# Performance work log

Measured on AMD Instinct MI355X. Metric: run time of the kernel, lower is better.

## Reference

```python
import jax, jax.numpy as jnp
import numpy as np

B, S, E = 4, 2048, 1024
H, DK = 16, 64

def setup_inputs() -> dict:
    key = jax.random.key(0)
    ks = jax.random.split(key, 9)
    sc = 1.0 / np.sqrt(E)
    return {
        "q": jax.random.normal(ks[0], (B, S, E), jnp.float32),
        "Wq": jax.random.normal(ks[1], (E, H * DK), jnp.float32) * sc,
        "bq": jax.random.normal(ks[2], (H * DK,), jnp.float32) * 0.01,
        "Wk": jax.random.normal(ks[3], (E, H * DK), jnp.float32) * sc,
        "bk": jax.random.normal(ks[4], (H * DK,), jnp.float32) * 0.01,
        "Wv": jax.random.normal(ks[5], (E, H * DK), jnp.float32) * sc,
        "bv": jax.random.normal(ks[6], (H * DK,), jnp.float32) * 0.01,
        "Wo": jax.random.normal(ks[7], (H * DK, E), jnp.float32) * sc,
        "bo": jax.random.normal(ks[8], (E,), jnp.float32) * 0.01,
    }

def _split_heads(x):
    # (B, S, H*DK) -> (B, H, S, DK)
    return x.reshape(B, S, H, DK).transpose(0, 2, 1, 3)

def reference(q, Wq, bq, Wk, bk, Wv, bv, Wo, bo):
    # self-attention: k = v = q (torch module path when k=v=None)
    qh = _split_heads(q @ Wq + bq)
    kh = _split_heads(q @ Wk + bk)
    vh = _split_heads(q @ Wv + bv)
    scale = 1.0 / jnp.sqrt(jnp.asarray(DK, qh.dtype))
    scores = jnp.einsum("bhqd,bhkd->bhqk", qh, kh) * scale  # (B,H,S,S)
    attn = jax.nn.softmax(scores, axis=-1)
    ctx = jnp.einsum("bhqk,bhkd->bhqd", attn, vh)
    ctx = ctx.transpose(0, 2, 1, 3).reshape(B, S, H * DK)
    return ctx @ Wo + bo
```

## Files before the change

kernel.cpp:

```cpp
#include <hip/hip_runtime.h>
#include <hip/hip_bf16.h>
#include <math.h>


typedef _Float16 f16x8 __attribute__((ext_vector_type(8)));
typedef _Float16 f16x4 __attribute__((ext_vector_type(4)));
typedef _Float16 f16x2 __attribute__((ext_vector_type(2)));
typedef float    f32x4 __attribute__((ext_vector_type(4)));
typedef unsigned int u32x2 __attribute__((ext_vector_type(2)));
typedef unsigned int u32x4 __attribute__((ext_vector_type(4)));

#define MFMA16(a,b,c) __builtin_amdgcn_mfma_f32_16x16x32_f16(a,b,c,0,0,0)

__device__ __forceinline__ void async_cp16(const _Float16* g, _Float16* l) {
    __builtin_amdgcn_global_load_lds(
        (const __attribute__((address_space(1))) unsigned int*)g,
        (__attribute__((address_space(3))) unsigned int*)l,
        16, 0, 0);
}

__device__ __forceinline__ f16x2 pk(float a, float b) {
    return __builtin_bit_cast(f16x2, __builtin_amdgcn_cvt_pkrtz(a, b));
}

__global__ void __launch_bounds__(256) prep_weights(
    const float* __restrict__ Wq, const float* __restrict__ Wk,
    const float* __restrict__ Wv, const float* __restrict__ Wo,
    _Float16* __restrict__ wt)
{
    __shared__ float tile[32][33];
    int mat = blockIdx.y;
    const float* W = (mat==0)?Wq:(mat==1)?Wk:(mat==2)?Wv:Wo;
    _Float16* WT = wt + (size_t)mat*1048576;
    int t = blockIdx.x;
    int kb = (t & 31) * 32;
    int nb = (t >> 5) * 32;
    int tx = threadIdx.x & 31, ty = threadIdx.x >> 5;
    #pragma unroll
    for (int r = 0; r < 4; ++r) {
        int row = ty + r*8;
        tile[row][tx] = W[(size_t)(kb+row)*1024 + nb + tx];
    }
    __syncthreads();
    #pragma unroll
    for (int r = 0; r < 4; ++r) {
        int row = ty + r*8;
        WT[(size_t)(nb+row)*1024 + kb + tx] = (_Float16)tile[tx][row];
    }
}

__global__ void __launch_bounds__(256) cvt_x(
    const float* __restrict__ X, _Float16* __restrict__ Xh)
{
    int i = (blockIdx.x*256 + threadIdx.x)*4;
    f32x4 x = *(const f32x4*)&X[i];
    f16x4 h;
    #pragma unroll
    for (int k=0;k<4;k++) h[k] = (_Float16)x[k];
    *(f16x4*)&Xh[i] = h;
}

__device__ __forceinline__ void stage3a(
    const _Float16* __restrict__ Ag, const _Float16* __restrict__ Bg, int kb,
    _Float16* sAb, _Float16* sBb, int wave, int lane)
{
    #pragma unroll
    for (int j = 0; j < 2; ++j) {
        int d   = j*512 + wave*64 + lane;
        int row = d >> 3;
        int sg  = (d & 7) ^ (row & 7);
        async_cp16(&Ag[(size_t)row*1024 + kb + sg*8], sAb + (j*512 + wave*64)*8);
    }
    {
        int d   = wave*64 + lane;
        int row = d >> 3;
        int sg  = (d & 7) ^ (row & 7);
        async_cp16(&Bg[(size_t)row*1024 + kb + sg*8], sBb + (wave*64)*8);
    }
}
__device__ __forceinline__ void stage3b(
    const _Float16* __restrict__ Bg, int kb, _Float16* sBb, int wave, int lane)
{
    #pragma unroll
    for (int j = 1; j < 4; ++j) {
        int d   = j*512 + wave*64 + lane;
        int row = d >> 3;
        int sg  = (d & 7) ^ (row & 7);
        async_cp16(&Bg[(size_t)row*1024 + kb + sg*8], sBb + (j*512 + wave*64)*8);
    }
}

#define GEMM_PIPE_LOOP()                                                       \
    stage3a(Ag, Bg, 0,  pA0, pB0, wave, lane);                                 \
    stage3b(Bg, 0,  pB0, wave, lane);                                          \
    stage3a(Ag, Bg, 64, pA1, pB1, wave, lane);                                 \
    stage3b(Bg, 64, pB1, wave, lane);                                          \
    asm volatile("s_waitcnt vmcnt(6)" ::: "memory");                           \
    __builtin_amdgcn_s_barrier();                                              \
    __builtin_amdgcn_sched_barrier(0);                                         \
    for (int t = 0; t < 16; ++t) {                                             \
                    \
        f16x8 af0[4], bf0[4];                                                  \
        _Pragma("unroll")                                                      \
        for (int i = 0; i < 4; ++i)                                            \
            af0[i] = *(const f16x8*)&pA0[(wr*64+i*16+cc)*64 +                  \
                                         ((q4^(cc&7))*8)];                     \
        _Pragma("unroll")                                                      \
        for (int j = 0; j < 4; ++j)                                            \
            bf0[j] = *(const f16x8*)&pB0[(wc*64+j*16+cc)*64 +                  \
                                         ((q4^(cc&7))*8)];                     \
        if (t < 14) stage3a(Ag, Bg, (t+2)*64, pA2, pB2, wave, lane);           \
        __builtin_amdgcn_sched_barrier(0);                                     \
        __builtin_amdgcn_s_barrier();                                          \
        asm volatile("s_waitcnt lgkmcnt(0)" ::: "memory");                     \
        __builtin_amdgcn_sched_barrier(0);                                     \
        __builtin_amdgcn_s_setprio(1);                                         \
        _Pragma("unroll")                                                      \
        for (int i = 0; i < 4; ++i)                                            \
            _Pragma("unroll")                                                  \
            for (int j = 0; j < 4; ++j)                                        \
                acc[i][j] = MFMA16(af0[i], bf0[j], acc[i][j]);                 \
        __builtin_amdgcn_s_setprio(0);                                         \
        __builtin_amdgcn_sched_barrier(0);                                     \
        __builtin_amdgcn_s_barrier();                                          \
            \
        f16x8 af1[4], bf1[4];                                                  \
        _Pragma("unroll")                                                      \
        for (int i = 0; i < 4; ++i)                                            \
            af1[i] = *(const f16x8*)&pA0[(wr*64+i*16+cc)*64 +                  \
                                         (((4+q4)^(cc&7))*8)];                 \
        _Pragma("unroll")                                                      \
        for (int j = 0; j < 4; ++j)                                            \
            bf1[j] = *(const f16x8*)&pB0[(wc*64+j*16+cc)*64 +                  \
                                         (((4+q4)^(cc&7))*8)];                 \
        if (t < 14) stage3b(Bg, (t+2)*64, pB2, wave, lane);                    \
        __builtin_amdgcn_sched_barrier(0);                                     \
        __builtin_amdgcn_s_barrier();                                          \
        asm volatile("s_waitcnt lgkmcnt(0)" ::: "memory");                     \
        __builtin_amdgcn_sched_barrier(0);                                     \
        __builtin_amdgcn_s_setprio(1);                                         \
        _Pragma("unroll")                                                      \
        for (int i = 0; i < 4; ++i)                                            \
            _Pragma("unroll")                                                  \
            for (int j = 0; j < 4; ++j)                                        \
                acc[i][j] = MFMA16(af1[i], bf1[j], acc[i][j]);                 \
        __builtin_amdgcn_s_setprio(0);                                         \
        if (t < 14) asm volatile("s_waitcnt vmcnt(6)" ::: "memory");           \
        else        asm volatile("s_waitcnt vmcnt(0)" ::: "memory");           \
        __builtin_amdgcn_sched_barrier(0);                                     \
        __builtin_amdgcn_s_barrier();                                          \
        _Float16* tA = pA0; pA0 = pA1; pA1 = pA2; pA2 = tA;                    \
        _Float16* tB = pB0; pB0 = pB1; pB1 = pB2; pB2 = tB;                    \
    }

__global__ void __launch_bounds__(512) gemm_qkv(
    const _Float16* __restrict__ Xh, const _Float16* __restrict__ wt,
    const float* __restrict__ bq, const float* __restrict__ bk, const float* __restrict__ bv,
    _Float16* __restrict__ Q, _Float16* __restrict__ K, _Float16* __restrict__ Vt)
{
    __shared__ __align__(16) _Float16 sA[3][8192];
    __shared__ __align__(16) _Float16 sB[3][16384];

    const int id = blockIdx.x;
    const int msub = id & 7;
    const int t2 = id >> 3;
    const int nblk = t2 % 12;
    const int mblk = (t2 / 12) * 8 + msub;

    const int tid = threadIdx.x;
    const int wave = tid >> 6, lane = tid & 63;
    const int wr = wave & 1, wc = wave >> 1;
    const int q4 = lane >> 4, cc = lane & 15;

    const int mat = nblk >> 2;
    const int colbase = (nblk & 3) * 256;
    const _Float16* Bg = wt + (size_t)mat*1048576 + (size_t)colbase*1024;
    const _Float16* Ag = Xh + (size_t)mblk*131072;

    _Float16 *pA0 = &sA[0][0], *pA1 = &sA[1][0], *pA2 = &sA[2][0];
    _Float16 *pB0 = &sB[0][0], *pB1 = &sB[1][0], *pB2 = &sB[2][0];

    f32x4 acc[4][4] = {};

    GEMM_PIPE_LOOP()

    const float* bias = (mat==0)?bq:(mat==1)?bk:bv;
    const float QSCALE = 0.125f * 1.44269504f;
    #pragma unroll
    for (int i=0;i<4;i++)
      #pragma unroll
      for (int j=0;j<4;j++)
        #pragma unroll
        for (int r=0;r<4;r++){
            int m = mblk*128 + wr*64 + i*16 + q4*4 + r;
            int ncol = colbase + wc*64 + j*16 + cc;
            float val = acc[i][j][r] + bias[ncol];
            int b = m >> 11, s = m & 2047;
            int h = ncol >> 6, dk = ncol & 63;
            if (mat == 2) {
                Vt[((size_t)(b*16+h)*64 + dk)*2048 + s] = (_Float16)val;
            } else {
                size_t qi = ((size_t)(b*16+h)*2048 + s)*64 + dk;
                if (mat == 0) Q[qi] = (_Float16)(val * QSCALE);
                else          K[qi] = (_Float16)val;
            }
        }
}

__global__ void __launch_bounds__(512) gemm_out(
    const _Float16* __restrict__ Ctx, const _Float16* __restrict__ wt,
    const float* __restrict__ bo,
    float* __restrict__ out)
{
    __shared__ __align__(16) _Float16 sA[3][8192];
    __shared__ __align__(16) _Float16 sB[3][16384];

    const int id = blockIdx.x;
    const int msub = id & 7;
    const int t2 = id >> 3;
    const int nblk = t2 & 3;
    const int mblk = (t2 >> 2) * 8 + msub;

    const int tid = threadIdx.x;
    const int wave = tid >> 6, lane = tid & 63;
    const int wr = wave & 1, wc = wave >> 1;
    const int q4 = lane >> 4, cc = lane & 15;

    const _Float16* Bg = wt + (size_t)3*1048576 + (size_t)nblk*256*1024;
    const _Float16* Ag = Ctx + (size_t)mblk*131072;

    _Float16 *pA0 = &sA[0][0], *pA1 = &sA[1][0], *pA2 = &sA[2][0];
    _Float16 *pB0 = &sB[0][0], *pB1 = &sB[1][0], *pB2 = &sB[2][0];

    f32x4 acc[4][4] = {};

    GEMM_PIPE_LOOP()

    #pragma unroll
    for (int i=0;i<4;i++)
      #pragma unroll
      for (int j=0;j<4;j++)
        #pragma unroll
        for (int r=0;r<4;r++){
            int m = mblk*128 + wr*64 + i*16 + q4*4 + r;
            int n = nblk*256 + wc*64 + j*16 + cc;
            out[(size_t)m*1024 + n] = acc[i][j][r] + bo[n];
        }
}

__global__ void __launch_bounds__(256,3) attn(
    const _Float16* __restrict__ Qg, const _Float16* __restrict__ Kg,
    const _Float16* __restrict__ Vg,
    _Float16* __restrict__ Ctx)
{
    __shared__ __align__(16) _Float16 sK[128][72];
    __shared__ __align__(16) _Float16 sV[64][136];

    const int id = blockIdx.x;
    const int xcd = id & 7;
    const int t2 = id >> 3;
    const int qc = t2 & 15;
    const int bh = (t2 >> 4) * 8 + xcd;

    const int tid = threadIdx.x;
    const int wave = tid >> 6, lane = tid & 63;
    const int q4 = lane >> 4, cc = lane & 15;

    const size_t hoff = (size_t)bh * 131072;
    const _Float16* Qp = Qg + hoff;
    const _Float16* Kp = Kg + hoff;
    const _Float16* Vp = Vg + hoff;

    const int qbase = qc*128 + wave*32;

    f16x8 qf[2][2];
    #pragma unroll
    for (int m=0;m<2;m++)
      #pragma unroll
      for (int ks=0;ks<2;ks++)
        qf[m][ks] = *(const f16x8*)&Qp[(qbase+m*16+cc)*64 + ks*32 + q4*8];

    f32x4 o[2][4] = {};
    float lsum[2] = {0.f, 0.f};

    const int r0 = tid >> 3, c8 = (tid & 7)*8;
    const int vrow = tid >> 4, vg = (tid & 15)*8;

    f16x8 kr[4], vr[4];
    #pragma unroll
    for (int p=0;p<4;p++){
        kr[p] = *(const f16x8*)&Kp[(p*32 + r0)*64 + c8];
        vr[p] = *(const f16x8*)&Vp[(size_t)(p*16 + vrow)*2048 + vg];
    }

    for (int kt = 0; kt < 16; ++kt) {
        __syncthreads();
        #pragma unroll
        for (int p=0;p<4;p++){
            *(f16x8*)&sK[p*32+r0][c8] = kr[p];
            *(f16x8*)&sV[p*16+vrow][vg] = vr[p];
        }
        __syncthreads();
        if (kt < 15) {
            #pragma unroll
            for (int p=0;p<4;p++){
                kr[p] = *(const f16x8*)&Kp[((kt+1)*128 + p*32 + r0)*64 + c8];
                vr[p] = *(const f16x8*)&Vp[(size_t)(p*16 + vrow)*2048 + (kt+1)*128 + vg];
            }
        }

        #pragma unroll
        for (int ks=0;ks<4;ks++){
            unsigned Ud[2][2], Wd[2][2];
            #pragma unroll
            for (int aa=0;aa<2;aa++){
                int kj = ks*2 + aa;
                f16x8 k0 = *(const f16x8*)&sK[kj*16+cc][q4*8];
                f16x8 k1 = *(const f16x8*)&sK[kj*16+cc][32+q4*8];
                #pragma unroll
                for (int m=0;m<2;m++){
                    f32x4 z = {};
                    f32x4 s = MFMA16(k0, qf[m][0], z);
                    s = MFMA16(k1, qf[m][1], s);
                    float p0 = __builtin_amdgcn_exp2f(s[0]);
                    float p1 = __builtin_amdgcn_exp2f(s[1]);
                    float p2 = __builtin_amdgcn_exp2f(s[2]);
                    float p3 = __builtin_amdgcn_exp2f(s[3]);
                    lsum[m] += (p0 + p1) + (p2 + p3);
                    unsigned d0 = __builtin_bit_cast(unsigned, pk(p0, p1));
                    unsigned d1 = __builtin_bit_cast(unsigned, pk(p2, p3));
                    if (aa == 0) { Ud[m][0] = d0; Ud[m][1] = d1; }
                    else         { Wd[m][0] = d0; Wd[m][1] = d1; }
                }
            }
            f16x8 pa[2];
            #pragma unroll
            for (int m=0;m<2;m++){
                u32x2 x0 = __builtin_amdgcn_permlane32_swap(Ud[m][0], Wd[m][0], false, false);
                u32x2 r02 = __builtin_amdgcn_permlane16_swap(x0[0], x0[1], false, false);
                u32x2 x1 = __builtin_amdgcn_permlane32_swap(Ud[m][1], Wd[m][1], false, false);
                u32x2 r13 = __builtin_amdgcn_permlane16_swap(x1[0], x1[1], false, false);
                u32x4 pw;
                pw[0] = r02[0]; pw[1] = r13[0]; pw[2] = r02[1]; pw[3] = r13[1];
                pa[m] = __builtin_bit_cast(f16x8, pw);
            }
            #pragma unroll
            for (int v=0;v<4;v++){
                f16x8 vf = *(const f16x8*)&sV[v*16+cc][ks*32+q4*8];
                o[0][v] = MFMA16(pa[0], vf, o[0][v]);
                o[1][v] = MFMA16(pa[1], vf, o[1][v]);
            }
        }
    }

    #pragma unroll
    for (int m=0;m<2;m++){
        lsum[m] += __shfl_xor(lsum[m], 16, 64);
        lsum[m] += __shfl_xor(lsum[m], 32, 64);
    }
    __syncthreads();
    float* sL = (float*)&sK[0][0];
    if (q4 == 0) {
        sL[wave*32 + cc]      = lsum[0];
        sL[wave*32 + 16 + cc] = lsum[1];
    }
    __syncthreads();

    int b = bh >> 4, h = bh & 15;
    #pragma unroll
    for (int m=0;m<2;m++)
      #pragma unroll
      for (int r=0;r<4;r++){
        float inv = 1.f / sL[wave*32 + m*16 + q4*4 + r];
        int s = qbase + m*16 + q4*4 + r;
        #pragma unroll
        for (int v=0;v<4;v++){
            float val = o[m][v][r]*inv;
            int dk = v*16 + cc;
            Ctx[((size_t)(b*2048+s)*16 + h)*64 + dk] = (_Float16)val;
        }
      }
}

extern "C" void kernel_launch(void* const* d_in, const int* in_sizes, int n_in,
                              void* d_out, int out_size, void* d_ws, size_t ws_size,
                              hipStream_t stream)
{
    const float* q  = (const float*)d_in[0];
    const float* Wq = (const float*)d_in[1];
    const float* bq = (const float*)d_in[2];
    const float* Wk = (const float*)d_in[3];
    const float* bk = (const float*)d_in[4];
    const float* Wv = (const float*)d_in[5];
    const float* bv = (const float*)d_in[6];
    const float* Wo = (const float*)d_in[7];
    const float* bo = (const float*)d_in[8];
    float* out = (float*)d_out;

    _Float16* ws  = (_Float16*)d_ws;
    _Float16* wt  = ws;
    _Float16* Xh  = ws + 4194304;
    _Float16* Q   = ws + 12582912;
    _Float16* K   = ws + 20971520;
    _Float16* Vt  = ws + 29360128;
    _Float16* Ctx = Xh;

    prep_weights<<<dim3(1024,4), 256, 0, stream>>>(Wq, Wk, Wv, Wo, wt);
    cvt_x<<<dim3(8192), 256, 0, stream>>>(q, Xh);
    gemm_qkv<<<dim3(768), 512, 0, stream>>>(Xh, wt, bq, bk, bv, Q, K, Vt);
    attn<<<dim3(1024), 256, 0, stream>>>(Q, K, Vt, Ctx);
    gemm_out<<<dim3(256), 512, 0, stream>>>(Ctx, wt, bo, out);
}
```

Before: 303.8 us.

## Double-buffer attention K/V tiles with async LDS loads and swizzle; remap GEMM blocks

The attention kernel stops staging K/V through registers. It now uses direct global-to-LDS async copies into a double-buffered, XOR-swizzled shared layout, with the K-tile size halved to 64 keys and twice as many iterations. This removes the register round-trip and the extra barrier per tile, and the swizzle avoids LDS bank conflicts without padding. The QKV and output GEMMs also get a new block-index mapping that groups M blocks per XCD into 4x4 tiles for better L2 reuse. The risks are more barriers from the smaller tiles and a full vmcnt(0) wait each iteration, which limits overlap.

```diff
diff --git a/kernel.cpp b/kernel.cpp
--- a/kernel.cpp
+++ b/kernel.cpp
@@ -162,10 +162,16 @@
     __shared__ __align__(16) _Float16 sB[3][16384];
 
     const int id = blockIdx.x;
-    const int msub = id & 7;
-    const int t2 = id >> 3;
-    const int nblk = t2 % 12;
-    const int mblk = (t2 / 12) * 8 + msub;
+    const int xcd = id & 7;
+    const int lid = id >> 3;
+    const int ng  = lid >> 5;
+    const int rem = lid & 31;
+    const int mq  = rem >> 4;
+    const int r2  = rem & 15;
+    const int m_lo = r2 >> 2;
+    const int nb   = r2 & 3;
+    const int mblk = (mq*4 + m_lo)*8 + xcd;
+    const int nblk = ng*4 + nb;
 
     const int tid = threadIdx.x;
     const int wave = tid >> 6, lane = tid & 63;
@@ -216,10 +222,13 @@
     __shared__ __align__(16) _Float16 sB[3][16384];
 
     const int id = blockIdx.x;
-    const int msub = id & 7;
-    const int t2 = id >> 3;
-    const int nblk = t2 & 3;
-    const int mblk = (t2 >> 2) * 8 + msub;
+    const int xcd = id & 7;
+    const int lid = id >> 3;
+    const int mq  = lid >> 4;
+    const int r2  = lid & 15;
+    const int m_lo = r2 >> 2;
+    const int nblk = r2 & 3;
+    const int mblk = (mq*4 + m_lo)*8 + xcd;
 
     const int tid = threadIdx.x;
     const int wave = tid >> 6, lane = tid & 63;
@@ -253,8 +262,9 @@
     const _Float16* __restrict__ Vg,
     _Float16* __restrict__ Ctx)
 {
-    __shared__ __align__(16) _Float16 sK[128][72];
-    __shared__ __align__(16) _Float16 sV[64][136];
+    __shared__ __align__(16) _Float16 sK[2][4096];
+    __shared__ __align__(16) _Float16 sV[2][4096];
+    __shared__ float sL[128];
 
     const int id = blockIdx.x;
     const int xcd = id & 7;
@@ -283,40 +293,64 @@
     f32x4 o[2][4] = {};
     float lsum[2] = {0.f, 0.f};
 
-    const int r0 = tid >> 3, c8 = (tid & 7)*8;
-    const int vrow = tid >> 4, vg = (tid & 15)*8;
-
-    f16x8 kr[4], vr[4];
-    #pragma unroll
-    for (int p=0;p<4;p++){
-        kr[p] = *(const f16x8*)&Kp[(p*32 + r0)*64 + c8];
-        vr[p] = *(const f16x8*)&Vp[(size_t)(p*16 + vrow)*2048 + vg];
-    }
-
-    for (int kt = 0; kt < 16; ++kt) {
-        __syncthreads();
-        #pragma unroll
-        for (int p=0;p<4;p++){
-            *(f16x8*)&sK[p*32+r0][c8] = kr[p];
-            *(f16x8*)&sV[p*16+vrow][vg] = vr[p];
-        }
-        __syncthreads();
-        if (kt < 15) {
+    const int srow = tid >> 3;
+    const int scg  = ((tid & 7) ^ ((tid >> 3) & 7)) * 8;
+    int kofs[2], vofs[2], dofs[2];
+    #pragma unroll
+    for (int rr = 0; rr < 2; ++rr) {
+        kofs[rr] = (rr*32 + srow)*64 + scg;
+        vofs[rr] = (rr*32 + srow)*2048 + scg;
+        dofs[rr] = rr*2048 + wave*512;
+    }
+    int okA[4], okB[4];
+    #pragma unroll
+    for (int kj=0;kj<4;kj++){
+        okA[kj] = (kj*16+cc)*64 + ((q4    ^(cc&7))*8);
+        okB[kj] = (kj*16+cc)*64 + (((4+q4)^(cc&7))*8);
+    }
+    int ov[2][4];
+    #pragma unroll
+    for (int ks=0;ks<2;ks++)
+      #pragma unroll
+      for (int v=0;v<4;v++)
+        ov[ks][v] = (v*16+cc)*64 + (((ks*4+q4)^(cc&7))*8);
+
+    #pragma unroll
+    for (int rr = 0; rr < 2; ++rr) {
+        async_cp16(Kp + kofs[rr], &sK[0][dofs[rr]]);
+        async_cp16(Vp + vofs[rr], &sV[0][dofs[rr]]);
+    }
+    asm volatile("s_waitcnt vmcnt(0)" ::: "memory");
+    __syncthreads();
+    __builtin_amdgcn_sched_barrier(0);
+
+    const _Float16* KbN = Kp + 4096;
+    const _Float16* VbN = Vp + 64;
+
+    #pragma unroll 2
+    for (int kt = 0; kt < 32; ++kt) {
+        const int cur = kt & 1;
+        const _Float16* kc = &sK[cur][0];
+        const _Float16* vc = &sV[cur][0];
+
+        if (kt < 31) {
+            _Float16* kn = &sK[cur ^ 1][0];
+            _Float16* vn = &sV[cur ^ 1][0];
             #pragma unroll
-            for (int p=0;p<4;p++){
-                kr[p] = *(const f16x8*)&Kp[((kt+1)*128 + p*32 + r0)*64 + c8];
-                vr[p] = *(const f16x8*)&Vp[(size_t)(p*16 + vrow)*2048 + (kt+1)*128 + vg];
+            for (int rr = 0; rr < 2; ++rr) {
+                async_cp16(KbN + kofs[rr], kn + dofs[rr]);
+                async_cp16(VbN + vofs[rr], vn + dofs[rr]);
             }
         }
 
         #pragma unroll
-        for (int ks=0;ks<4;ks++){
+        for (int ks=0;ks<2;ks++){
             unsigned Ud[2][2], Wd[2][2];
             #pragma unroll
             for (int aa=0;aa<2;aa++){
                 int kj = ks*2 + aa;
-                f16x8 k0 = *(const f16x8*)&sK[kj*16+cc][q4*8];
-                f16x8 k1 = *(const f16x8*)&sK[kj*16+cc][32+q4*8];
+                f16x8 k0 = *(const f16x8*)&kc[okA[kj]];
+                f16x8 k1 = *(const f16x8*)&kc[okB[kj]];
                 #pragma unroll
                 for (int m=0;m<2;m++){
                     f32x4 z = {};
@@ -346,11 +380,17 @@
             }
             #pragma unroll
             for (int v=0;v<4;v++){
-                f16x8 vf = *(const f16x8*)&sV[v*16+cc][ks*32+q4*8];
+                f16x8 vf = *(const f16x8*)&vc[ov[ks][v]];
                 o[0][v] = MFMA16(pa[0], vf, o[0][v]);
                 o[1][v] = MFMA16(pa[1], vf, o[1][v]);
             }
         }
+
+        KbN += 4096;
+        VbN += 64;
+        asm volatile("s_waitcnt vmcnt(0)" ::: "memory");
+        __syncthreads();
+        __builtin_amdgcn_sched_barrier(0);
     }
 
     #pragma unroll
@@ -358,8 +398,6 @@
         lsum[m] += __shfl_xor(lsum[m], 16, 64);
         lsum[m] += __shfl_xor(lsum[m], 32, 64);
     }
-    __syncthreads();
-    float* sL = (float*)&sK[0][0];
     if (q4 == 0) {
         sL[wave*32 + cc]      = lsum[0];
         sL[wave*32 + 16 + cc] = lsum[1];
```

Measured after the change: 292.9 us. -3.6%, faster.
